# Kernel optimization log

Measured on AMD Instinct MI355X. Metric: run time of the kernel, lower is better.

## Reference

```python
import jax, jax.numpy as jnp
import numpy as np
from jax import lax

N_IMG = 2
LEVEL_HW = [(200, 200), (100, 100), (50, 50), (25, 25), (13, 13)]
STRIDES = [4, 8, 16, 32, 64]
SIZES = [32.0, 64.0, 128.0, 256.0, 512.0]
A = 3
LEVEL_SIZES = [A * h * w for h, w in LEVEL_HW]
R = sum(LEVEL_SIZES)  # 159882
PRE_NMS = 1000   # pre_nms_top_n['testing']
POST_NMS = 1000  # post_nms_top_n['testing']
NMS_THRESH = 0.7
SCORE_THRESH = 0.0
MIN_SIZE = 1e-3
IMG_H = IMG_W = 800.0
BBOX_XFORM_CLIP = float(np.log(1000.0 / 16.0))


def _make_anchors():
    ratios = np.array([0.5, 1.0, 2.0])
    h_r = np.sqrt(ratios)
    w_r = 1.0 / h_r
    out = []
    for (h, w), stride, size in zip(LEVEL_HW, STRIDES, SIZES):
        ws = size * w_r
        hs = size * h_r
        base = np.stack([-ws / 2, -hs / 2, ws / 2, hs / 2], 1)  # [A,4]
        sx = (np.arange(w) + 0.5) * stride
        sy = (np.arange(h) + 0.5) * stride
        yy, xx = np.meshgrid(sy, sx, indexing='ij')
        shifts = np.stack([xx.ravel(), yy.ravel(), xx.ravel(), yy.ravel()], 1)  # [H*W,4]
        out.append((shifts[:, None, :] + base[None, :, :]).reshape(-1, 4))
    return np.concatenate(out, 0).astype(np.float32)  # [R,4]


def setup_inputs() -> dict:
    key = jax.random.key(0)
    k1, k2 = jax.random.split(key)
    objectness = jax.random.normal(k1, (N_IMG, R), jnp.float32)
    deltas = jax.random.normal(k2, (N_IMG, R, 4), jnp.float32) * 0.2
    anchors = jnp.asarray(_make_anchors())
    return {"objectness": objectness, "deltas": deltas, "anchors": anchors}


def _decode(deltas, anchors):
    # BoxCoder.decode with weights (1,1,1,1)
    wa = anchors[:, 2] - anchors[:, 0]
    ha = anchors[:, 3] - anchors[:, 1]
    cxa = anchors[:, 0] + 0.5 * wa
    cya = anchors[:, 1] + 0.5 * ha
    dx, dy, dw, dh = deltas[..., 0], deltas[..., 1], deltas[..., 2], deltas[..., 3]
    dw = jnp.minimum(dw, BBOX_XFORM_CLIP)
    dh = jnp.minimum(dh, BBOX_XFORM_CLIP)
    cx = dx * wa + cxa
    cy = dy * ha + cya
    w = jnp.exp(dw) * wa
    h = jnp.exp(dh) * ha
    return jnp.stack([cx - 0.5 * w, cy - 0.5 * h, cx + 0.5 * w, cy + 0.5 * h], -1)


def _nms_single(boxes, scores, lvl, valid):
    # batched_nms via per-level coordinate offset trick
    offs = lvl.astype(boxes.dtype) * (max(IMG_H, IMG_W) + 1.0)
    ob = boxes + offs[:, None]
    s = jnp.where(valid, scores, -1.0)
    order = jnp.argsort(-s)
    b = ob[order]          # offset boxes, score-descending
    raw = boxes[order]     # original boxes
    v = valid[order]
    ss = s[order]
    area = (b[:, 2] - b[:, 0]) * (b[:, 3] - b[:, 1])
    lt = jnp.maximum(b[:, None, :2], b[None, :, :2])
    rb = jnp.minimum(b[:, None, 2:], b[None, :, 2:])
    wh = jnp.clip(rb - lt, 0.0)
    inter = wh[..., 0] * wh[..., 1]
    iou = inter / (area[:, None] + area[None, :] - inter + 1e-9)  # [K,K]
    K = b.shape[0]

    def body(keep, i):
        suppressed = jnp.any(keep & (iou[:, i] > NMS_THRESH))
        keep = keep.at[i].set(v[i] & ~suppressed)
        return keep, None

    keep, _ = lax.scan(body, jnp.zeros((K,), bool), jnp.arange(K))
    # compact kept boxes (score order preserved) into fixed POST_NMS slots
    pos = jnp.where(keep, jnp.minimum(jnp.cumsum(keep) - 1, POST_NMS), POST_NMS)
    out_b = jnp.zeros((POST_NMS + 1, 4), boxes.dtype).at[pos].set(raw)[:POST_NMS]
    out_s = jnp.full((POST_NMS + 1,), -1.0, boxes.dtype).at[pos].set(ss)[:POST_NMS]
    return out_b, out_s


def _forward(objectness, deltas, anchors):
    proposals = _decode(deltas, anchors)  # [N,R,4]
    # per-level topk (pre_nms_top_n)
    idxs = []
    off = 0
    for n in LEVEL_SIZES:
        k = min(PRE_NMS, n)
        _, ti = lax.top_k(objectness[:, off:off + n], k)
        idxs.append(ti + off)
        off += n
    top_idx = jnp.concatenate(idxs, 1)  # [N,K]
    obj = jnp.take_along_axis(objectness, top_idx, 1)
    boxes = jnp.take_along_axis(proposals, top_idx[..., None], 1)
    levels = jnp.concatenate([jnp.full((n,), i, jnp.int32) for i, n in enumerate(LEVEL_SIZES)])
    lvl = levels[top_idx]
    scores = jax.nn.sigmoid(obj)
    # clip_boxes_to_image
    x1 = jnp.clip(boxes[..., 0], 0.0, IMG_W)
    y1 = jnp.clip(boxes[..., 1], 0.0, IMG_H)
    x2 = jnp.clip(boxes[..., 2], 0.0, IMG_W)
    y2 = jnp.clip(boxes[..., 3], 0.0, IMG_H)
    boxes = jnp.stack([x1, y1, x2, y2], -1)
    # remove_small_boxes + score_thresh -> validity mask (fixed shapes)
    valid = (x2 - x1 >= MIN_SIZE) & (y2 - y1 >= MIN_SIZE) & (scores >= SCORE_THRESH)
    return jax.vmap(_nms_single)(boxes, scores, lvl, valid)


def reference(objectness, deltas, anchors):
    return _forward(objectness, deltas, anchors)
```

## Files before the change

kernel.cpp:

```cpp
#include <hip/hip_runtime.h>

typedef unsigned long long u64;
typedef unsigned int u32;

#define R_TOT 159882
#define POST 1000
#define IMG_SZ 800.0f
#define NMS_TH 0.7f
#define BBOX_CLIP 4.135166556742356f
#define LCAP 1024

__device__ __forceinline__ float fadd_(float a, float b){ return __fadd_rn(a,b); }
__device__ __forceinline__ float fsub_(float a, float b){ return __fsub_rn(a,b); }
__device__ __forceinline__ float fmul_(float a, float b){ return __fmul_rn(a,b); }

__device__ __forceinline__ int lvl_len(int l){ const int L[5]={120000,30000,7500,1875,507}; return L[l]; }
__device__ __forceinline__ int lvl_off(int l){ const int L[5]={0,120000,150000,157500,159375}; return L[l]; }
__device__ __forceinline__ int lvl_k(int l){ const int L[5]={1000,1000,1000,1000,507}; return L[l]; }

__device__ __forceinline__ u32 mono_(u32 u){ return (u & 0x80000000u) ? ~u : (u | 0x80000000u); }

__device__ __forceinline__ u64 readlane64(u64 v, int i){
  u32 lo = (u32)__builtin_amdgcn_readlane((int)(u32)v, i);
  u32 hi = (u32)__builtin_amdgcn_readlane((int)(u32)(v >> 32), i);
  return ((u64)hi << 32) | (u64)lo;
}

__global__ __launch_bounds__(256) void k_hist(const float* __restrict__ obj, int* hist16,
                                              int* cntg, int* cnt2){
  int g = blockIdx.x, sl = blockIdx.y;
  int img = g/5, lvl = g%5;
  int n = lvl_len(lvl), s0 = lvl_off(lvl);
  __shared__ int lh[4096];
  int tid = threadIdx.x;
  for (int i = tid; i < 4096; i += 256) lh[i] = 0;
  if (sl == 0 && tid == 0){ cntg[g] = 0; cnt2[g] = 0; }
  __syncthreads();
  int lo = (int)((long long)n * sl / 16), hiS = (int)((long long)n * (sl+1) / 16);
  const float* p = obj + img*R_TOT + s0;
  #pragma unroll 4
  for (int e = lo + tid; e < hiS; e += 256){
    u32 mu = mono_(__float_as_uint(p[e]));
    atomicAdd(&lh[(~mu) >> 20], 1);
  }
  __syncthreads();
  int* dst = hist16 + (g*16 + sl)*4096;
  for (int i = tid; i < 4096; i += 256) dst[i] = lh[i];
}

__global__ __launch_bounds__(256) void k_collect(const float* __restrict__ obj,
                                                 const int* __restrict__ hist16,
                                                 int* bstarG, int* remG,
                                                 int* cntg, int* cnt2,
                                                 u64* mainG, u64* LbufG){
  int g = blockIdx.x, sl = blockIdx.y;
  int img = g/5, lvl = g%5;
  int n = lvl_len(lvl), s0 = lvl_off(lvl), k = lvl_k(lvl);
  int tid = threadIdx.x, lane = tid & 63, wid = tid >> 6;
  __shared__ int wsum[4];
  __shared__ int sh_bs, sh_rem;
  __shared__ int lc, lc2, gbase, gbase2;
  __shared__ u64 lmain[1024];
  __shared__ u64 lbuf2[1024];

  int h[16];
  #pragma unroll
  for (int j = 0; j < 16; j++) h[j] = 0;
  const int* hb = hist16 + g*16*4096 + 16*tid;
  for (int s2 = 0; s2 < 16; s2++){
    const int4* hs = (const int4*)(hb + s2*4096);
    int4 a = hs[0], b = hs[1], c = hs[2], d = hs[3];
    h[0]+=a.x;  h[1]+=a.y;  h[2]+=a.z;  h[3]+=a.w;
    h[4]+=b.x;  h[5]+=b.y;  h[6]+=b.z;  h[7]+=b.w;
    h[8]+=c.x;  h[9]+=c.y;  h[10]+=c.z; h[11]+=c.w;
    h[12]+=d.x; h[13]+=d.y; h[14]+=d.z; h[15]+=d.w;
  }
  int part = 0;
  #pragma unroll
  for (int j = 0; j < 16; j++) part += h[j];
  int x = part;
  for (int d = 1; d < 64; d <<= 1){ int y = __shfl_up(x, d); if (lane >= d) x += y; }
  if (lane == 63) wsum[wid] = x;
  if (tid == 0){ lc = 0; lc2 = 0; }
  __syncthreads();
  int add = 0;
  for (int w = 0; w < wid; w++) add += wsum[w];
  int incl = x + add, excl = incl - part;
  if (excl < k && k <= incl){
    int cum = excl;
    #pragma unroll
    for (int q = 0; q < 16; q++){
      if (cum + h[q] >= k){ sh_bs = 16*tid + q; sh_rem = k - cum; break; }
      cum += h[q];
    }
  }
  __syncthreads();
  int bs = sh_bs;
  if (sl == 0 && tid == 0){ bstarG[g] = bs; remG[g] = sh_rem; }

  int lo = (int)((long long)n * sl / 16), hiS = (int)((long long)n * (sl+1) / 16);
  const float* p = obj + img*R_TOT + s0;
  #pragma unroll 4
  for (int e = lo + tid; e < hiS; e += 256){
    u32 mu = mono_(__float_as_uint(p[e]));
    u64 key56 = (((u64)(~mu)) << 24) | (u32)(s0 + e);
    int bin = (int)(key56 >> 44);
    if (bin < bs){ int pos = atomicAdd(&lc, 1); lmain[pos] = key56; }
    else if (bin == bs){ int pos = atomicAdd(&lc2, 1); if (pos < 1024) lbuf2[pos] = key56; }
  }
  __syncthreads();
  if (tid == 0){ gbase = atomicAdd(&cntg[g], lc); gbase2 = atomicAdd(&cnt2[g], lc2); }
  __syncthreads();
  int b1 = gbase, c1 = lc;
  for (int i = tid; i < c1; i += 256) mainG[g*1024 + b1 + i] = lmain[i];
  int b2 = gbase2, c2l = lc2 < 1024 ? lc2 : 1024;
  for (int i = tid; i < c2l; i += 256){
    int gp = b2 + i;
    if (gp < LCAP) LbufG[g*LCAP + gp] = lbuf2[i];
  }
}

__global__ __launch_bounds__(1024) void k_seldecode(const float* __restrict__ obj,
                                                    const float4* __restrict__ deltas,
                                                    const float4* __restrict__ anchors,
                                                    const u64* __restrict__ mainG,
                                                    const u64* __restrict__ LbufG,
                                                    const int* __restrict__ cntg,
                                                    const int* __restrict__ cnt2,
                                                    const int* __restrict__ remG,
                                                    const int* __restrict__ bstarG,
                                                    float4* boxL, float* scoreL,
                                                    float4* nbox, u64* okeyN, int* ncnt){
  int g = blockIdx.x, img = g/5, lvl = g%5;
  int s0 = lvl_off(lvl), n = lvl_len(lvl), k = lvl_k(lvl);
  const float* p = obj + img*R_TOT + s0;
  __shared__ u64 Lbuf[LCAP];
  __shared__ u64 mainL[1024];
  __shared__ float4 lbox[1024];
  __shared__ u64 lokey[1024];
  __shared__ unsigned char lval[1024];
  __shared__ int h16[16];
  __shared__ int sh_sc, sh_rem;
  __shared__ u64 sh_thr;
  int tid = threadIdx.x, lane = tid & 63;
  int nb = cntg[g];
  int c2 = cnt2[g];
  int rem = remG[g];
  int bs = bstarG[g];
  mainL[tid] = (tid < nb) ? mainG[g*1024 + tid] : ~0ull;
  if (tid == 0){ sh_sc = 0; sh_rem = rem; }
  int c2c = c2 < LCAP ? c2 : LCAP;
  for (int e = tid; e < c2c; e += 1024) Lbuf[e] = LbufG[g*LCAP + e];
  __syncthreads();
  if (c2 <= LCAP){
    for (int e = tid; e < c2; e += 1024){
      u64 kk = Lbuf[e];
      int rk = 0;
      for (int q = 0; q < c2; q++) rk += (Lbuf[q] < kk) ? 1 : 0;
      if (rk < rem){ int p2 = atomicAdd(&sh_sc, 1); mainL[nb + p2] = kk; }
    }
  } else {
    if (tid == 0) sh_thr = ((u64)bs) << 44;
    __syncthreads();
    for (int shift = 40; shift >= 0; shift -= 4){
      if (tid < 16) h16[tid] = 0;
      __syncthreads();
      u64 pref = sh_thr;
      u64 himask = ~((1ull << (shift+4)) - 1ull);
      for (int e = tid; e < n; e += 1024){
        u32 mu = mono_(__float_as_uint(p[e]));
        u64 kk = (((u64)(~mu)) << 24) | (u32)(s0 + e);
        if ((kk & himask) == (pref & himask)) atomicAdd(&h16[(int)((kk >> shift) & 15)], 1);
      }
      __syncthreads();
      if (tid == 0){
        int r2 = sh_rem, cum = 0;
        for (int d = 0; d < 16; d++){
          int hb = h16[d];
          if (cum + hb >= r2){ sh_thr = pref | ((u64)d << shift); sh_rem = r2 - cum; break; }
          cum += hb;
        }
      }
      __syncthreads();
    }
    u64 thr = sh_thr;
    for (int e = tid; e < n; e += 1024){
      u32 mu = mono_(__float_as_uint(p[e]));
      u64 kk = (((u64)(~mu)) << 24) | (u32)(s0 + e);
      if ((int)(kk >> 44) == bs && kk <= thr){ int p2 = atomicAdd(&sh_sc, 1); mainL[nb + p2] = kk; }
    }
  }
  __syncthreads();
  for (int k2 = 2; k2 <= 1024; k2 <<= 1){
    for (int j = k2 >> 1; j > 0; j >>= 1){
      __syncthreads();
      int i = tid, ixj = i ^ j;
      if (ixj > i){
        u64 a = mainL[i], b = mainL[ixj];
        bool up = (i & k2) == 0;
        if ((a > b) == up){ mainL[i] = b; mainL[ixj] = a; }
      }
    }
  }
  __syncthreads();
  int r = tid, t = g*1024 + r;
  if (r < k){
    int idx = (int)(mainL[r] & 0xFFFFFFu);
    float4 a = anchors[idx];
    float4 d = deltas[img*R_TOT + idx];
    float o = obj[img*R_TOT + idx];
    float wa = fsub_(a.z, a.x), ha = fsub_(a.w, a.y);
    float cxa = fadd_(a.x, fmul_(0.5f, wa)), cya = fadd_(a.y, fmul_(0.5f, ha));
    float dw = fminf(d.z, BBOX_CLIP), dh = fminf(d.w, BBOX_CLIP);
    float cx = fadd_(fmul_(d.x, wa), cxa), cy = fadd_(fmul_(d.y, ha), cya);
    float w  = fmul_(expf(dw), wa),        h  = fmul_(expf(dh), ha);
    float x1 = fsub_(cx, fmul_(0.5f, w)), y1 = fsub_(cy, fmul_(0.5f, h));
    float x2 = fadd_(cx, fmul_(0.5f, w)), y2 = fadd_(cy, fmul_(0.5f, h));
    x1 = fminf(fmaxf(x1, 0.0f), IMG_SZ); y1 = fminf(fmaxf(y1, 0.0f), IMG_SZ);
    x2 = fminf(fmaxf(x2, 0.0f), IMG_SZ); y2 = fminf(fmaxf(y2, 0.0f), IMG_SZ);
    bool valid = (fsub_(x2, x1) >= 1e-3f) && (fsub_(y2, y1) >= 1e-3f);
    float e = expf(-o);
    float sig = __fdiv_rn(1.0f, fadd_(1.0f, e));
    float s = valid ? sig : -1.0f;
    u32 sb = __float_as_uint(s);
    u32 ms = (sb & 0x80000000u) ? ~sb : (sb | 0x80000000u);
    float4 b4 = make_float4(x1, y1, x2, y2);
    boxL[t] = b4;
    scoreL[t] = sig;
    lokey[r] = (((u64)(~ms)) << 32) | (u32)(lvl*1000 + r);
    lbox[r] = b4;
    lval[r] = valid ? 1 : 0;
  } else {
    lval[r] = 0;
  }
  __syncthreads();
  if (tid < 64){
    int cnt = 0;
    float off = (float)lvl * 801.0f;
    for (int base = 0; base < k; base += 64){
      int r2 = base + lane;
      bool v = (r2 < k) && lval[r2];
      float4 b = lbox[r2 < k ? r2 : 0];
      u64 mask = __ballot(v);
      int before = __popcll(mask & ((1ull << lane) - 1ull));
      if (v){
        int pos = cnt + before;
        nbox[g*1024 + pos] = make_float4(fadd_(b.x,off), fadd_(b.y,off), fadd_(b.z,off), fadd_(b.w,off));
        okeyN[g*1024 + pos] = lokey[r2];
      }
      cnt += __popcll(mask);
    }
    if (lane == 0) ncnt[g] = cnt;
  }
}

__global__ __launch_bounds__(64) void k_mask(const float4* __restrict__ nbox,
                                             const int* __restrict__ ncnt,
                                             u64* LTG2){
  int g = blockIdx.x, tr = blockIdx.y, tw = blockIdx.z;
  if (tw > tr) return;
  int m = ncnt[g];
  if (tr*64 >= m) return;
  __shared__ float4 shb[64];
  int lane = threadIdx.x;
  if (tw*64 + lane < m) shb[lane] = nbox[g*1024 + tw*64 + lane];
  __syncthreads();
  int j = tr*64 + lane;
  if (j >= m) return;
  float4 a = nbox[g*1024 + j];
  float areaA = fmul_(fsub_(a.z,a.x), fsub_(a.w,a.y));
  int imax = m - tw*64; if (imax > 64) imax = 64;
  if (tw == tr){
    u64 bitsF = 0;
    for (int ii = lane+1; ii < imax; ii++){
      float4 b = shb[ii];
      float ltx = fmaxf(a.x, b.x), lty = fmaxf(a.y, b.y);
      float rbx = fminf(a.z, b.z), rby = fminf(a.w, b.w);
      float wx = fmaxf(fsub_(rbx, ltx), 0.0f), wy = fmaxf(fsub_(rby, lty), 0.0f);
      float inter = fmul_(wx, wy);
      float areaB = fmul_(fsub_(b.z,b.x), fsub_(b.w,b.y));
      float den = fadd_(fsub_(fadd_(areaA, areaB), inter), 1e-9f);
      if (__fdiv_rn(inter, den) > NMS_TH) bitsF |= (1ull << ii);
    }
    LTG2[((size_t)(g*1024 + j))*16 + 15] = bitsF;
  } else {
    u64 bits = 0;
    for (int ii = 0; ii < imax; ii++){
      float4 b = shb[ii];
      float ltx = fmaxf(a.x, b.x), lty = fmaxf(a.y, b.y);
      float rbx = fminf(a.z, b.z), rby = fminf(a.w, b.w);
      float wx = fmaxf(fsub_(rbx, ltx), 0.0f), wy = fmaxf(fsub_(rby, lty), 0.0f);
      float inter = fmul_(wx, wy);
      float areaB = fmul_(fsub_(b.z,b.x), fsub_(b.w,b.y));
      float den = fadd_(fsub_(fadd_(areaA, areaB), inter), 1e-9f);
      if (__fdiv_rn(inter, den) > NMS_TH) bits |= (1ull << ii);
    }
    LTG2[((size_t)(g*1024 + j))*16 + tw] = bits;
  }
}

__device__ __forceinline__ int lbound(const u64* a, int n, u64 key){
  int lo = 0, hi = n;
  while (lo < hi){ int mid = (lo + hi) >> 1; if (a[mid] < key) lo = mid + 1; else hi = mid; }
  return lo;
}

struct ChunkBuf {
  ulonglong2 v0, v1, v2, v3, v4, v5, v6, v7;
  u64 ok;
};

__device__ __forceinline__ void issue_chunk(const u64* __restrict__ LT2,
                                            const u64* __restrict__ oK,
                                            int c, int lane, ChunkBuf& b){
  int row = c*64 + lane;
  const ulonglong2* rp = (const ulonglong2*)(LT2 + (size_t)row*16);
  b.v0 = rp[0]; b.v1 = rp[1]; b.v2 = rp[2]; b.v3 = rp[3];
  b.v4 = rp[4]; b.v5 = rp[5]; b.v6 = rp[6]; b.v7 = rp[7];
  b.ok = oK[row];
}

__device__ __forceinline__ void consume_chunk(const ChunkBuf& b, int c, int m, int lane,
                                              u64* KwR, u64* runsL, int& cnt){
  int row = c*64 + lane;
  bool inr = row < m;
  u64 supp = 0;
  #define TERM(q, val) supp |= (((q) < c) ? (val) : 0ull) & KwR[q];
  TERM(0,  b.v0.x) TERM(1,  b.v0.y) TERM(2,  b.v1.x) TERM(3,  b.v1.y)
  TERM(4,  b.v2.x) TERM(5,  b.v2.y) TERM(6,  b.v3.x) TERM(7,  b.v3.y)
  TERM(8,  b.v4.x) TERM(9,  b.v4.y) TERM(10, b.v5.x) TERM(11, b.v5.y)
  TERM(12, b.v6.x) TERM(13, b.v6.y) TERM(14, b.v7.x)
  #undef TERM
  u64 fwd = inr ? b.v7.y : 0;
  u64 live = __ballot(inr && (supp == 0));
  u64 fz = __ballot(fwd != 0);
  u64 kept = 0;
  while (1){
    u64 lf = live & fz;
    if (!lf){ kept |= live; break; }
    int i = __builtin_ctzll(lf);
    u64 bi = 1ull << i;
    u64 below = live & (bi - 1ull);
    kept |= below | bi;
    live &= ~(below | bi);
    live &= ~readlane64(fwd, i);
  }
  KwR[c] = kept;
  bool kp = (kept >> lane) & 1ull;
  int before = __popcll(kept & ((1ull << lane) - 1ull));
  if (kp) runsL[cnt + before] = b.ok;
  cnt += __popcll(kept);
}

__global__ __launch_bounds__(1024) void k_scanmerge(const u64* __restrict__ LTG2,
                                                    const int* __restrict__ ncnt,
                                                    const u64* __restrict__ okeyN,
                                                    const float4* __restrict__ boxL,
                                                    const float* __restrict__ scoreL,
                                                    float* out){
  int img = blockIdx.x, tid = threadIdx.x, lane = tid & 63, wid = tid >> 6;
  __shared__ u64 runs[5*1024];
  __shared__ u64 Kw[5][16];
  __shared__ int cl[5];
  if (wid < 5){
    int l = wid, g = img*5 + l;
    int m = ncnt[g];
    int nch = (m + 63) >> 6;
    const u64* LT2 = LTG2 + ((size_t)g*1024)*16;
    const u64* oK = okeyN + g*1024;
    u64* KwR = &Kw[l][0];
    u64* runsL = &runs[l*1024];
    int cnt = 0;
    ChunkBuf A, B;
    if (nch > 0){
      issue_chunk(LT2, oK, 0, lane, A);
      int c = 0;
      while (c < nch){
        if (c+1 < nch) issue_chunk(LT2, oK, c+1, lane, B);
        consume_chunk(A, c, m, lane, KwR, runsL, cnt);
        c++;
        if (c >= nch) break;
        if (c+1 < nch) issue_chunk(LT2, oK, c+1, lane, A);
        consume_chunk(B, c, m, lane, KwR, runsL, cnt);
        c++;
      }
    }
    if (lane == 0) cl[l] = cnt;
  } else {
    for (int t = tid - 320; t < POST; t += 704){
      out[img*POST*4 + t*4 + 0] = 0.0f;
      out[img*POST*4 + t*4 + 1] = 0.0f;
      out[img*POST*4 + t*4 + 2] = 0.0f;
      out[img*POST*4 + t*4 + 3] = 0.0f;
      out[2*POST*4 + img*POST + t] = -1.0f;
    }
  }
  __syncthreads();
  for (int idx = tid; idx < 5*1024; idx += 1024){
    int l = idx >> 10, i = idx & 1023;
    if (i < cl[l]){
      u64 key = runs[l*1024 + i];
      int o0 = l+1; if (o0 >= 5) o0 -= 5;
      int o1 = l+2; if (o1 >= 5) o1 -= 5;
      int o2 = l+3; if (o2 >= 5) o2 -= 5;
      int o3 = l+4; if (o3 >= 5) o3 -= 5;
      const u64* r0 = runs + (o0 << 10);
      const u64* r1 = runs + (o1 << 10);
      const u64* r2 = runs + (o2 << 10);
      const u64* r3 = runs + (o3 << 10);
      int lo0 = 0, hi0 = cl[o0];
      int lo1 = 0, hi1 = cl[o1];
      int lo2 = 0, hi2 = cl[o2];
      int lo3 = 0, hi3 = cl[o3];
      #pragma unroll 1
      for (int st = 0; st < 11; st++){
        int m0 = (lo0+hi0)>>1, m1 = (lo1+hi1)>>1, m2 = (lo2+hi2)>>1, m3 = (lo3+hi3)>>1;
        u64 a0 = r0[m0], a1 = r1[m1], a2 = r2[m2], a3 = r3[m3];
        if (lo0 < hi0){ if (a0 < key) lo0 = m0+1; else hi0 = m0; }
        if (lo1 < hi1){ if (a1 < key) lo1 = m1+1; else hi1 = m1; }
        if (lo2 < hi2){ if (a2 < key) lo2 = m2+1; else hi2 = m2; }
        if (lo3 < hi3){ if (a3 < key) lo3 = m3+1; else hi3 = m3; }
      }
      int rank = i + lo0 + lo1 + lo2 + lo3;
      if (rank < POST){
        int pos = (int)(key & 0xFFFFFFFFull);
        int lvl = pos / 1000, r = pos - lvl*1000;
        int gg = img*5 + lvl;
        float4 bo = boxL[gg*1024 + r];
        float sc = scoreL[gg*1024 + r];
        out[img*POST*4 + rank*4 + 0] = bo.x;
        out[img*POST*4 + rank*4 + 1] = bo.y;
        out[img*POST*4 + rank*4 + 2] = bo.z;
        out[img*POST*4 + rank*4 + 3] = bo.w;
        out[2*POST*4 + img*POST + rank] = sc;
      }
    }
  }
}

extern "C" void kernel_launch(void* const* d_in, const int* in_sizes, int n_in,
                              void* d_out, int out_size, void* d_ws, size_t ws_size,
                              hipStream_t stream){
  (void)in_sizes; (void)n_in; (void)out_size; (void)ws_size;
  const float*  obj     = (const float*)d_in[0];
  const float4* deltas  = (const float4*)d_in[1];
  const float4* anchors = (const float4*)d_in[2];
  float* out = (float*)d_out;
  char* ws = (char*)d_ws;
  int* hist16  = (int*)(ws + 0);
  int* bstarG  = (int*)(ws + 2621440);
  int* remG    = (int*)(ws + 2621696);
  int* cntg    = (int*)(ws + 2621952);
  int* cnt2    = (int*)(ws + 2622208);
  u64* mainG   = (u64*)(ws + 2622464);
  u64* LbufG   = (u64*)(ws + 2704384);
  float4* boxL = (float4*)(ws + 2786304);
  float* scoreL= (float*)(ws + 2950144);
  u64* okeyN   = (u64*)(ws + 2991104);
  float4* nbox = (float4*)(ws + 3073024);
  u64* LTG2    = (u64*)(ws + 3236864);
  int* ncnt    = (int*)(ws + 4547584);

  {
    dim3 gh(10, 16);
    k_hist<<<gh, 256, 0, stream>>>(obj, hist16, cntg, cnt2);
  }
  {
    dim3 gc(10, 16);
    k_collect<<<gc, 256, 0, stream>>>(obj, hist16, bstarG, remG, cntg, cnt2, mainG, LbufG);
  }
  k_seldecode<<<10, 1024, 0, stream>>>(obj, deltas, anchors, mainG, LbufG, cntg, cnt2,
                                       remG, bstarG, boxL, scoreL, nbox, okeyN, ncnt);
  {
    dim3 gm(10, 16, 16);
    k_mask<<<gm, 64, 0, stream>>>(nbox, ncnt, LTG2);
  }
  k_scanmerge<<<2, 1024, 0, stream>>>(LTG2, ncnt, okeyN, boxL, scoreL, out);
}
```

Measured before the change: 157.6 us.

## Fuse per-level NMS into selection kernel with lazy suppression against kept boxes

Merges the IoU mask kernel and the per-level greedy scan into the selection/decode kernel, so the boxes stay in shared memory and there is no global IoU bitmask. Each chunk's suppression is now computed on demand: each wave checks the current chunk's rows only against boxes already kept in earlier chunks, stopping at the first overlap. The within-chunk diagonal mask is still precomputed. This drops one kernel launch, the upper-triangular IoU work and the global traffic for the mask. In exchange it adds a serial loop with two block barriers per chunk inside a 10-block kernel, which leaves little parallelism on the GPU.

```diff
diff --git a/kernel.cpp b/kernel.cpp
--- a/kernel.cpp
+++ b/kernel.cpp
@@ -120,29 +120,34 @@
   }
 }
 
-__global__ __launch_bounds__(1024) void k_seldecode(const float* __restrict__ obj,
-                                                    const float4* __restrict__ deltas,
-                                                    const float4* __restrict__ anchors,
-                                                    const u64* __restrict__ mainG,
-                                                    const u64* __restrict__ LbufG,
-                                                    const int* __restrict__ cntg,
-                                                    const int* __restrict__ cnt2,
-                                                    const int* __restrict__ remG,
-                                                    const int* __restrict__ bstarG,
-                                                    float4* boxL, float* scoreL,
-                                                    float4* nbox, u64* okeyN, int* ncnt){
+__global__ __launch_bounds__(1024) void k_selnms(const float* __restrict__ obj,
+                                                 const float4* __restrict__ deltas,
+                                                 const float4* __restrict__ anchors,
+                                                 const u64* __restrict__ mainG,
+                                                 const u64* __restrict__ LbufG,
+                                                 const int* __restrict__ cntg,
+                                                 const int* __restrict__ cnt2,
+                                                 const int* __restrict__ remG,
+                                                 const int* __restrict__ bstarG,
+                                                 float4* boxL, float* scoreL,
+                                                 u64* keptK, int* kcnt){
   int g = blockIdx.x, img = g/5, lvl = g%5;
   int s0 = lvl_off(lvl), n = lvl_len(lvl), k = lvl_k(lvl);
   const float* p = obj + img*R_TOT + s0;
+  __shared__ u64 mainL[1024];
   __shared__ u64 Lbuf[LCAP];
-  __shared__ u64 mainL[1024];
   __shared__ float4 lbox[1024];
   __shared__ u64 lokey[1024];
   __shared__ unsigned char lval[1024];
+  __shared__ float4 cbox[1024];
   __shared__ int h16[16];
-  __shared__ int sh_sc, sh_rem;
+  __shared__ int sh_sc, sh_rem, sh_m;
   __shared__ u64 sh_thr;
-  int tid = threadIdx.x, lane = tid & 63;
+  __shared__ u64 Kw[16];
+  __shared__ u64 suppW[16];
+  u64* diagL = mainL;
+  u64* ckey  = Lbuf;
+  int tid = threadIdx.x, lane = tid & 63, wid = tid >> 6;
   int nb = cntg[g];
   int c2 = cnt2[g];
   int rem = remG[g];
@@ -245,146 +250,110 @@
       int before = __popcll(mask & ((1ull << lane) - 1ull));
       if (v){
         int pos = cnt + before;
-        nbox[g*1024 + pos] = make_float4(fadd_(b.x,off), fadd_(b.y,off), fadd_(b.z,off), fadd_(b.w,off));
-        okeyN[g*1024 + pos] = lokey[r2];
+        cbox[pos] = make_float4(fadd_(b.x,off), fadd_(b.y,off), fadd_(b.z,off), fadd_(b.w,off));
+        ckey[pos] = lokey[r2];
       }
       cnt += __popcll(mask);
     }
-    if (lane == 0) ncnt[g] = cnt;
-  }
-}
-
-__global__ __launch_bounds__(64) void k_mask(const float4* __restrict__ nbox,
-                                             const int* __restrict__ ncnt,
-                                             u64* LTG2){
-  int g = blockIdx.x, tr = blockIdx.y, tw = blockIdx.z;
-  if (tw > tr) return;
-  int m = ncnt[g];
-  if (tr*64 >= m) return;
-  __shared__ float4 shb[64];
-  int lane = threadIdx.x;
-  if (tw*64 + lane < m) shb[lane] = nbox[g*1024 + tw*64 + lane];
-  __syncthreads();
-  int j = tr*64 + lane;
-  if (j >= m) return;
-  float4 a = nbox[g*1024 + j];
-  float areaA = fmul_(fsub_(a.z,a.x), fsub_(a.w,a.y));
-  int imax = m - tw*64; if (imax > 64) imax = 64;
-  if (tw == tr){
-    u64 bitsF = 0;
-    for (int ii = lane+1; ii < imax; ii++){
-      float4 b = shb[ii];
-      float ltx = fmaxf(a.x, b.x), lty = fmaxf(a.y, b.y);
-      float rbx = fminf(a.z, b.z), rby = fminf(a.w, b.w);
-      float wx = fmaxf(fsub_(rbx, ltx), 0.0f), wy = fmaxf(fsub_(rby, lty), 0.0f);
-      float inter = fmul_(wx, wy);
-      float areaB = fmul_(fsub_(b.z,b.x), fsub_(b.w,b.y));
-      float den = fadd_(fsub_(fadd_(areaA, areaB), inter), 1e-9f);
-      if (__fdiv_rn(inter, den) > NMS_TH) bitsF |= (1ull << ii);
-    }
-    LTG2[((size_t)(g*1024 + j))*16 + 15] = bitsF;
-  } else {
+    if (lane == 0) sh_m = cnt;
+  }
+  if (tid < 16) Kw[tid] = 0;
+  __syncthreads();
+  int m = sh_m;
+  int nch = (m + 63) >> 6;
+  {
+    int row = wid*64 + lane;
     u64 bits = 0;
-    for (int ii = 0; ii < imax; ii++){
-      float4 b = shb[ii];
-      float ltx = fmaxf(a.x, b.x), lty = fmaxf(a.y, b.y);
-      float rbx = fminf(a.z, b.z), rby = fminf(a.w, b.w);
-      float wx = fmaxf(fsub_(rbx, ltx), 0.0f), wy = fmaxf(fsub_(rby, lty), 0.0f);
-      float inter = fmul_(wx, wy);
-      float areaB = fmul_(fsub_(b.z,b.x), fsub_(b.w,b.y));
-      float den = fadd_(fsub_(fadd_(areaA, areaB), inter), 1e-9f);
-      if (__fdiv_rn(inter, den) > NMS_TH) bits |= (1ull << ii);
-    }
-    LTG2[((size_t)(g*1024 + j))*16 + tw] = bits;
-  }
-}
-
-__device__ __forceinline__ int lbound(const u64* a, int n, u64 key){
-  int lo = 0, hi = n;
-  while (lo < hi){ int mid = (lo + hi) >> 1; if (a[mid] < key) lo = mid + 1; else hi = mid; }
-  return lo;
-}
-
-struct ChunkBuf {
-  ulonglong2 v0, v1, v2, v3, v4, v5, v6, v7;
-  u64 ok;
-};
-
-__device__ __forceinline__ void issue_chunk(const u64* __restrict__ LT2,
-                                            const u64* __restrict__ oK,
-                                            int c, int lane, ChunkBuf& b){
-  int row = c*64 + lane;
-  const ulonglong2* rp = (const ulonglong2*)(LT2 + (size_t)row*16);
-  b.v0 = rp[0]; b.v1 = rp[1]; b.v2 = rp[2]; b.v3 = rp[3];
-  b.v4 = rp[4]; b.v5 = rp[5]; b.v6 = rp[6]; b.v7 = rp[7];
-  b.ok = oK[row];
-}
-
-__device__ __forceinline__ void consume_chunk(const ChunkBuf& b, int c, int m, int lane,
-                                              u64* KwR, u64* runsL, int& cnt){
-  int row = c*64 + lane;
-  bool inr = row < m;
-  u64 supp = 0;
-  #define TERM(q, val) supp |= (((q) < c) ? (val) : 0ull) & KwR[q];
-  TERM(0,  b.v0.x) TERM(1,  b.v0.y) TERM(2,  b.v1.x) TERM(3,  b.v1.y)
-  TERM(4,  b.v2.x) TERM(5,  b.v2.y) TERM(6,  b.v3.x) TERM(7,  b.v3.y)
-  TERM(8,  b.v4.x) TERM(9,  b.v4.y) TERM(10, b.v5.x) TERM(11, b.v5.y)
-  TERM(12, b.v6.x) TERM(13, b.v6.y) TERM(14, b.v7.x)
-  #undef TERM
-  u64 fwd = inr ? b.v7.y : 0;
-  u64 live = __ballot(inr && (supp == 0));
-  u64 fz = __ballot(fwd != 0);
-  u64 kept = 0;
-  while (1){
-    u64 lf = live & fz;
-    if (!lf){ kept |= live; break; }
-    int i = __builtin_ctzll(lf);
-    u64 bi = 1ull << i;
-    u64 below = live & (bi - 1ull);
-    kept |= below | bi;
-    live &= ~(below | bi);
-    live &= ~readlane64(fwd, i);
-  }
-  KwR[c] = kept;
-  bool kp = (kept >> lane) & 1ull;
-  int before = __popcll(kept & ((1ull << lane) - 1ull));
-  if (kp) runsL[cnt + before] = b.ok;
-  cnt += __popcll(kept);
-}
-
-__global__ __launch_bounds__(1024) void k_scanmerge(const u64* __restrict__ LTG2,
-                                                    const int* __restrict__ ncnt,
-                                                    const u64* __restrict__ okeyN,
-                                                    const float4* __restrict__ boxL,
-                                                    const float* __restrict__ scoreL,
-                                                    float* out){
+    if (wid < nch && row < m){
+      float4 a = cbox[row];
+      float areaA = fmul_(fsub_(a.z,a.x), fsub_(a.w,a.y));
+      int imax = m - wid*64; if (imax > 64) imax = 64;
+      for (int ii = lane+1; ii < imax; ii++){
+        float4 b = cbox[wid*64 + ii];
+        float ltx = fmaxf(a.x, b.x), lty = fmaxf(a.y, b.y);
+        float rbx = fminf(a.z, b.z), rby = fminf(a.w, b.w);
+        float wx = fmaxf(fsub_(rbx, ltx), 0.0f), wy = fmaxf(fsub_(rby, lty), 0.0f);
+        float inter = fmul_(wx, wy);
+        float areaB = fmul_(fsub_(b.z,b.x), fsub_(b.w,b.y));
+        float den = fadd_(fsub_(fadd_(areaA, areaB), inter), 1e-9f);
+        if (__fdiv_rn(inter, den) > NMS_TH) bits |= (1ull << ii);
+      }
+    }
+    diagL[wid*64 + lane] = bits;
+  }
+  __syncthreads();
+  int cnt = 0;
+  for (int c = 0; c < nch; c++){
+    bool sup = false;
+    if (wid < c){
+      u64 wk = Kw[wid];
+      int row = c*64 + lane;
+      if (wk && row < m){
+        float4 a = cbox[row];
+        float areaA = fmul_(fsub_(a.z,a.x), fsub_(a.w,a.y));
+        u64 w2 = wk;
+        while (w2){
+          int i = __builtin_ctzll(w2); w2 &= w2 - 1ull;
+          float4 b = cbox[wid*64 + i];
+          float ltx = fmaxf(a.x, b.x), lty = fmaxf(a.y, b.y);
+          float rbx = fminf(a.z, b.z), rby = fminf(a.w, b.w);
+          float wx = fmaxf(fsub_(rbx, ltx), 0.0f), wy = fmaxf(fsub_(rby, lty), 0.0f);
+          float inter = fmul_(wx, wy);
+          float areaB = fmul_(fsub_(b.z,b.x), fsub_(b.w,b.y));
+          float den = fadd_(fsub_(fadd_(areaA, areaB), inter), 1e-9f);
+          if (__fdiv_rn(inter, den) > NMS_TH){ sup = true; break; }
+        }
+      }
+      u64 pw = __ballot(sup);
+      if (lane == 0) suppW[wid] = pw;
+    } else {
+      if (wid < 16 && lane == 0) suppW[wid] = 0;
+    }
+    __syncthreads();
+    if (wid == 0){
+      u64 supp = 0;
+      #pragma unroll
+      for (int q = 0; q < 16; q++) supp |= suppW[q];
+      int row = c*64 + lane;
+      bool inr = row < m;
+      u64 fwd = diagL[row];
+      bool slane = (supp >> lane) & 1ull;
+      u64 live = __ballot(inr && !slane);
+      u64 fz = __ballot(fwd != 0);
+      u64 kept = 0;
+      while (1){
+        u64 lf = live & fz;
+        if (!lf){ kept |= live; break; }
+        int i = __builtin_ctzll(lf);
+        u64 bi = 1ull << i;
+        u64 below = live & (bi - 1ull);
+        kept |= below | bi;
+        live &= ~(below | bi);
+        live &= ~readlane64(fwd, i);
+      }
+      Kw[c] = kept;
+      bool kp = (kept >> lane) & 1ull;
+      int before = __popcll(kept & ((1ull << lane) - 1ull));
+      if (kp) keptK[g*1024 + cnt + before] = ckey[row];
+      cnt += __popcll(kept);
+    }
+    __syncthreads();
+  }
+  if (tid == 0) kcnt[g] = cnt;
+}
+
+__global__ __launch_bounds__(1024) void k_merge(const u64* __restrict__ keptK,
+                                                const int* __restrict__ kcnt,
+                                                const float4* __restrict__ boxL,
+                                                const float* __restrict__ scoreL,
+                                                float* out){
   int img = blockIdx.x, tid = threadIdx.x, lane = tid & 63, wid = tid >> 6;
   __shared__ u64 runs[5*1024];
-  __shared__ u64 Kw[5][16];
   __shared__ int cl[5];
   if (wid < 5){
     int l = wid, g = img*5 + l;
-    int m = ncnt[g];
-    int nch = (m + 63) >> 6;
-    const u64* LT2 = LTG2 + ((size_t)g*1024)*16;
-    const u64* oK = okeyN + g*1024;
-    u64* KwR = &Kw[l][0];
-    u64* runsL = &runs[l*1024];
-    int cnt = 0;
-    ChunkBuf A, B;
-    if (nch > 0){
-      issue_chunk(LT2, oK, 0, lane, A);
-      int c = 0;
-      while (c < nch){
-        if (c+1 < nch) issue_chunk(LT2, oK, c+1, lane, B);
-        consume_chunk(A, c, m, lane, KwR, runsL, cnt);
-        c++;
-        if (c >= nch) break;
-        if (c+1 < nch) issue_chunk(LT2, oK, c+1, lane, A);
-        consume_chunk(B, c, m, lane, KwR, runsL, cnt);
-        c++;
-      }
-    }
+    int cnt = kcnt[g];
+    for (int i = lane; i < cnt; i += 64) runs[l*1024 + i] = keptK[g*1024 + i];
     if (lane == 0) cl[l] = cnt;
   } else {
     for (int t = tid - 320; t < POST; t += 704){
@@ -456,10 +425,8 @@
   u64* LbufG   = (u64*)(ws + 2704384);
   float4* boxL = (float4*)(ws + 2786304);
   float* scoreL= (float*)(ws + 2950144);
-  u64* okeyN   = (u64*)(ws + 2991104);
-  float4* nbox = (float4*)(ws + 3073024);
-  u64* LTG2    = (u64*)(ws + 3236864);
-  int* ncnt    = (int*)(ws + 4547584);
+  u64* keptK   = (u64*)(ws + 2991104);
+  int* kcnt    = (int*)(ws + 3073024);
 
   {
     dim3 gh(10, 16);
@@ -469,11 +436,7 @@
     dim3 gc(10, 16);
     k_collect<<<gc, 256, 0, stream>>>(obj, hist16, bstarG, remG, cntg, cnt2, mainG, LbufG);
   }
-  k_seldecode<<<10, 1024, 0, stream>>>(obj, deltas, anchors, mainG, LbufG, cntg, cnt2,
-                                       remG, bstarG, boxL, scoreL, nbox, okeyN, ncnt);
-  {
-    dim3 gm(10, 16, 16);
-    k_mask<<<gm, 64, 0, stream>>>(nbox, ncnt, LTG2);
-  }
-  k_scanmerge<<<2, 1024, 0, stream>>>(LTG2, ncnt, okeyN, boxL, scoreL, out);
-}
+  k_selnms<<<10, 1024, 0, stream>>>(obj, deltas, anchors, mainG, LbufG, cntg, cnt2,
+                                    remG, bstarG, boxL, scoreL, keptK, kcnt);
+  k_merge<<<2, 1024, 0, stream>>>(keptK, kcnt, boxL, scoreL, out);
+}
```

Result: slower. 338.9 us (+115.1%).

## Fuse histogram, collect and select-decode into one per-level block kernel

Applied to the files above, without the earlier changes.

Merges the three top-k stages (sliced histogram, collect, select/decode) into a single kernel with one 1024-thread block per image-level. The global histogram slices, counters and candidate buffers go away and are replaced by shared memory, which removes two launches and the global round-trips between them. In exchange, each level is scanned twice by only 10 blocks instead of 160, so the large 120k level loses parallelism.

```diff
diff --git a/kernel.cpp b/kernel.cpp
--- a/kernel.cpp
+++ b/kernel.cpp
@@ -26,82 +26,61 @@
   return ((u64)hi << 32) | (u64)lo;
 }
 
-__global__ __launch_bounds__(256) void k_hist(const float* __restrict__ obj, int* hist16,
-                                              int* cntg, int* cnt2){
-  int g = blockIdx.x, sl = blockIdx.y;
-  int img = g/5, lvl = g%5;
-  int n = lvl_len(lvl), s0 = lvl_off(lvl);
+__global__ __launch_bounds__(1024) void k_select(const float* __restrict__ obj,
+                                                 const float4* __restrict__ deltas,
+                                                 const float4* __restrict__ anchors,
+                                                 float4* boxL, float* scoreL,
+                                                 float4* nbox, u64* okeyN, int* ncnt){
+  int g = blockIdx.x, img = g/5, lvl = g%5;
+  int s0 = lvl_off(lvl), n = lvl_len(lvl), k = lvl_k(lvl);
+  const float* p = obj + img*R_TOT + s0;
   __shared__ int lh[4096];
-  int tid = threadIdx.x;
-  for (int i = tid; i < 4096; i += 256) lh[i] = 0;
-  if (sl == 0 && tid == 0){ cntg[g] = 0; cnt2[g] = 0; }
-  __syncthreads();
-  int lo = (int)((long long)n * sl / 16), hiS = (int)((long long)n * (sl+1) / 16);
-  const float* p = obj + img*R_TOT + s0;
-  #pragma unroll 4
-  for (int e = lo + tid; e < hiS; e += 256){
+  __shared__ u64 lmain[1024];
+  __shared__ u64 lbuf2[1024];
+  __shared__ float4 lbox[1024];
+  __shared__ u64 lokey[1024];
+  __shared__ unsigned char lval[1024];
+  __shared__ int wsum[16];
+  __shared__ int h16[16];
+  __shared__ int sh_bs, sh_rem, sh_sc, lc, lc2;
+  __shared__ u64 sh_thr;
+  int tid = threadIdx.x, lane = tid & 63, wid = tid >> 6;
+
+  for (int i = tid; i < 4096; i += 1024) lh[i] = 0;
+  lmain[tid] = ~0ull;
+  if (tid == 0){ lc = 0; lc2 = 0; sh_sc = 0; }
+  __syncthreads();
+
+  for (int e = tid; e < n; e += 1024){
     u32 mu = mono_(__float_as_uint(p[e]));
     atomicAdd(&lh[(~mu) >> 20], 1);
   }
   __syncthreads();
-  int* dst = hist16 + (g*16 + sl)*4096;
-  for (int i = tid; i < 4096; i += 256) dst[i] = lh[i];
-}
-
-__global__ __launch_bounds__(256) void k_collect(const float* __restrict__ obj,
-                                                 const int* __restrict__ hist16,
-                                                 int* bstarG, int* remG,
-                                                 int* cntg, int* cnt2,
-                                                 u64* mainG, u64* LbufG){
-  int g = blockIdx.x, sl = blockIdx.y;
-  int img = g/5, lvl = g%5;
-  int n = lvl_len(lvl), s0 = lvl_off(lvl), k = lvl_k(lvl);
-  int tid = threadIdx.x, lane = tid & 63, wid = tid >> 6;
-  __shared__ int wsum[4];
-  __shared__ int sh_bs, sh_rem;
-  __shared__ int lc, lc2, gbase, gbase2;
-  __shared__ u64 lmain[1024];
-  __shared__ u64 lbuf2[1024];
-
-  int h[16];
-  #pragma unroll
-  for (int j = 0; j < 16; j++) h[j] = 0;
-  const int* hb = hist16 + g*16*4096 + 16*tid;
-  for (int s2 = 0; s2 < 16; s2++){
-    const int4* hs = (const int4*)(hb + s2*4096);
-    int4 a = hs[0], b = hs[1], c = hs[2], d = hs[3];
-    h[0]+=a.x;  h[1]+=a.y;  h[2]+=a.z;  h[3]+=a.w;
-    h[4]+=b.x;  h[5]+=b.y;  h[6]+=b.z;  h[7]+=b.w;
-    h[8]+=c.x;  h[9]+=c.y;  h[10]+=c.z; h[11]+=c.w;
-    h[12]+=d.x; h[13]+=d.y; h[14]+=d.z; h[15]+=d.w;
-  }
-  int part = 0;
-  #pragma unroll
-  for (int j = 0; j < 16; j++) part += h[j];
+
+  int h0 = lh[4*tid], h1 = lh[4*tid+1], h2 = lh[4*tid+2], h3 = lh[4*tid+3];
+  int part = h0 + h1 + h2 + h3;
   int x = part;
   for (int d = 1; d < 64; d <<= 1){ int y = __shfl_up(x, d); if (lane >= d) x += y; }
   if (lane == 63) wsum[wid] = x;
-  if (tid == 0){ lc = 0; lc2 = 0; }
   __syncthreads();
   int add = 0;
   for (int w = 0; w < wid; w++) add += wsum[w];
   int incl = x + add, excl = incl - part;
   if (excl < k && k <= incl){
     int cum = excl;
-    #pragma unroll
-    for (int q = 0; q < 16; q++){
-      if (cum + h[q] >= k){ sh_bs = 16*tid + q; sh_rem = k - cum; break; }
-      cum += h[q];
-    }
-  }
-  __syncthreads();
-  int bs = sh_bs;
-  if (sl == 0 && tid == 0){ bstarG[g] = bs; remG[g] = sh_rem; }
-
-  int lo = (int)((long long)n * sl / 16), hiS = (int)((long long)n * (sl+1) / 16);
-  const float* p = obj + img*R_TOT + s0;
-  #pragma unroll 4
-  for (int e = lo + tid; e < hiS; e += 256){
+    if (cum + h0 >= k){ sh_bs = 4*tid;   sh_rem = k - cum; }
+    else { cum += h0;
+      if (cum + h1 >= k){ sh_bs = 4*tid+1; sh_rem = k - cum; }
+      else { cum += h1;
+        if (cum + h2 >= k){ sh_bs = 4*tid+2; sh_rem = k - cum; }
+        else { cum += h2;    sh_bs = 4*tid+3; sh_rem = k - cum; }
+      }
+    }
+  }
+  __syncthreads();
+  int bs = sh_bs, rem0 = sh_rem;
+
+  for (int e = tid; e < n; e += 1024){
     u32 mu = mono_(__float_as_uint(p[e]));
     u64 key56 = (((u64)(~mu)) << 24) | (u32)(s0 + e);
     int bin = (int)(key56 >> 44);
@@ -109,55 +88,14 @@
     else if (bin == bs){ int pos = atomicAdd(&lc2, 1); if (pos < 1024) lbuf2[pos] = key56; }
   }
   __syncthreads();
-  if (tid == 0){ gbase = atomicAdd(&cntg[g], lc); gbase2 = atomicAdd(&cnt2[g], lc2); }
-  __syncthreads();
-  int b1 = gbase, c1 = lc;
-  for (int i = tid; i < c1; i += 256) mainG[g*1024 + b1 + i] = lmain[i];
-  int b2 = gbase2, c2l = lc2 < 1024 ? lc2 : 1024;
-  for (int i = tid; i < c2l; i += 256){
-    int gp = b2 + i;
-    if (gp < LCAP) LbufG[g*LCAP + gp] = lbuf2[i];
-  }
-}
-
-__global__ __launch_bounds__(1024) void k_seldecode(const float* __restrict__ obj,
-                                                    const float4* __restrict__ deltas,
-                                                    const float4* __restrict__ anchors,
-                                                    const u64* __restrict__ mainG,
-                                                    const u64* __restrict__ LbufG,
-                                                    const int* __restrict__ cntg,
-                                                    const int* __restrict__ cnt2,
-                                                    const int* __restrict__ remG,
-                                                    const int* __restrict__ bstarG,
-                                                    float4* boxL, float* scoreL,
-                                                    float4* nbox, u64* okeyN, int* ncnt){
-  int g = blockIdx.x, img = g/5, lvl = g%5;
-  int s0 = lvl_off(lvl), n = lvl_len(lvl), k = lvl_k(lvl);
-  const float* p = obj + img*R_TOT + s0;
-  __shared__ u64 Lbuf[LCAP];
-  __shared__ u64 mainL[1024];
-  __shared__ float4 lbox[1024];
-  __shared__ u64 lokey[1024];
-  __shared__ unsigned char lval[1024];
-  __shared__ int h16[16];
-  __shared__ int sh_sc, sh_rem;
-  __shared__ u64 sh_thr;
-  int tid = threadIdx.x, lane = tid & 63;
-  int nb = cntg[g];
-  int c2 = cnt2[g];
-  int rem = remG[g];
-  int bs = bstarG[g];
-  mainL[tid] = (tid < nb) ? mainG[g*1024 + tid] : ~0ull;
-  if (tid == 0){ sh_sc = 0; sh_rem = rem; }
-  int c2c = c2 < LCAP ? c2 : LCAP;
-  for (int e = tid; e < c2c; e += 1024) Lbuf[e] = LbufG[g*LCAP + e];
-  __syncthreads();
+  int nb = lc, c2 = lc2;
+
   if (c2 <= LCAP){
     for (int e = tid; e < c2; e += 1024){
-      u64 kk = Lbuf[e];
+      u64 kk = lbuf2[e];
       int rk = 0;
-      for (int q = 0; q < c2; q++) rk += (Lbuf[q] < kk) ? 1 : 0;
-      if (rk < rem){ int p2 = atomicAdd(&sh_sc, 1); mainL[nb + p2] = kk; }
+      for (int q = 0; q < c2; q++) rk += (lbuf2[q] < kk) ? 1 : 0;
+      if (rk < rem0){ int p2 = atomicAdd(&sh_sc, 1); lmain[nb + p2] = kk; }
     }
   } else {
     if (tid == 0) sh_thr = ((u64)bs) << 44;
@@ -187,25 +125,27 @@
     for (int e = tid; e < n; e += 1024){
       u32 mu = mono_(__float_as_uint(p[e]));
       u64 kk = (((u64)(~mu)) << 24) | (u32)(s0 + e);
-      if ((int)(kk >> 44) == bs && kk <= thr){ int p2 = atomicAdd(&sh_sc, 1); mainL[nb + p2] = kk; }
-    }
-  }
-  __syncthreads();
+      if ((int)(kk >> 44) == bs && kk <= thr){ int p2 = atomicAdd(&sh_sc, 1); lmain[nb + p2] = kk; }
+    }
+  }
+  __syncthreads();
+
   for (int k2 = 2; k2 <= 1024; k2 <<= 1){
     for (int j = k2 >> 1; j > 0; j >>= 1){
       __syncthreads();
       int i = tid, ixj = i ^ j;
       if (ixj > i){
-        u64 a = mainL[i], b = mainL[ixj];
+        u64 a = lmain[i], b = lmain[ixj];
         bool up = (i & k2) == 0;
-        if ((a > b) == up){ mainL[i] = b; mainL[ixj] = a; }
-      }
-    }
-  }
-  __syncthreads();
+        if ((a > b) == up){ lmain[i] = b; lmain[ixj] = a; }
+      }
+    }
+  }
+  __syncthreads();
+
   int r = tid, t = g*1024 + r;
   if (r < k){
-    int idx = (int)(mainL[r] & 0xFFFFFFu);
+    int idx = (int)(lmain[r] & 0xFFFFFFu);
     float4 a = anchors[idx];
     float4 d = deltas[img*R_TOT + idx];
     float o = obj[img*R_TOT + idx];
@@ -234,6 +174,7 @@
     lval[r] = 0;
   }
   __syncthreads();
+
   if (tid < 64){
     int cnt = 0;
     float off = (float)lvl * 801.0f;
@@ -297,12 +238,6 @@
     }
     LTG2[((size_t)(g*1024 + j))*16 + tw] = bits;
   }
-}
-
-__device__ __forceinline__ int lbound(const u64* a, int n, u64 key){
-  int lo = 0, hi = n;
-  while (lo < hi){ int mid = (lo + hi) >> 1; if (a[mid] < key) lo = mid + 1; else hi = mid; }
-  return lo;
 }
 
 struct ChunkBuf {
@@ -447,30 +382,14 @@
   const float4* anchors = (const float4*)d_in[2];
   float* out = (float*)d_out;
   char* ws = (char*)d_ws;
-  int* hist16  = (int*)(ws + 0);
-  int* bstarG  = (int*)(ws + 2621440);
-  int* remG    = (int*)(ws + 2621696);
-  int* cntg    = (int*)(ws + 2621952);
-  int* cnt2    = (int*)(ws + 2622208);
-  u64* mainG   = (u64*)(ws + 2622464);
-  u64* LbufG   = (u64*)(ws + 2704384);
-  float4* boxL = (float4*)(ws + 2786304);
-  float* scoreL= (float*)(ws + 2950144);
-  u64* okeyN   = (u64*)(ws + 2991104);
-  float4* nbox = (float4*)(ws + 3073024);
-  u64* LTG2    = (u64*)(ws + 3236864);
-  int* ncnt    = (int*)(ws + 4547584);
-
-  {
-    dim3 gh(10, 16);
-    k_hist<<<gh, 256, 0, stream>>>(obj, hist16, cntg, cnt2);
-  }
-  {
-    dim3 gc(10, 16);
-    k_collect<<<gc, 256, 0, stream>>>(obj, hist16, bstarG, remG, cntg, cnt2, mainG, LbufG);
-  }
-  k_seldecode<<<10, 1024, 0, stream>>>(obj, deltas, anchors, mainG, LbufG, cntg, cnt2,
-                                       remG, bstarG, boxL, scoreL, nbox, okeyN, ncnt);
+  float4* boxL = (float4*)(ws + 0);
+  float* scoreL= (float*)(ws + 163840);
+  u64* okeyN   = (u64*)(ws + 204800);
+  float4* nbox = (float4*)(ws + 286720);
+  u64* LTG2    = (u64*)(ws + 450560);
+  int* ncnt    = (int*)(ws + 1761280);
+
+  k_select<<<10, 1024, 0, stream>>>(obj, deltas, anchors, boxL, scoreL, nbox, okeyN, ncnt);
   {
     dim3 gm(10, 16, 16);
     k_mask<<<gm, 64, 0, stream>>>(nbox, ncnt, LTG2);
```

Result: slower. 195.4 us (+24.0%).
